# Performance work log

Hardware: AMD Instinct MI355X
Metric: run time of the kernel (lower is better)

## Reference

```python
import jax, jax.numpy as jnp
import numpy as np

B, N, D, H = 8, 8192, 512, 8  # batch, seq, hidden, heads
DH = D // H


def _rope_tables(n, d, dtype=jnp.float32):
    # standard rotate-half RoPE tables over the full hidden dim (d/2 freq pairs)
    half = d // 2
    inv_freq = 1.0 / (10000.0 ** (np.arange(0, half, dtype=np.float32) / half))
    pos = np.arange(n, dtype=np.float32)
    ang = np.einsum('n,f->nf', pos, inv_freq)          # [N, D/2]
    ang = np.concatenate([ang, ang], axis=-1)          # [N, D]
    return jnp.asarray(np.cos(ang), dtype), jnp.asarray(np.sin(ang), dtype)


def setup_inputs() -> dict:
    key = jax.random.key(0)
    k1, k2 = jax.random.split(key)
    hidden_states = jax.random.normal(k1, (B, N, D), dtype=jnp.float32)
    num_layers = 24
    std = 0.02 / np.sqrt(2.0 * num_layers * D)
    W = jax.random.normal(k2, (D, D), dtype=jnp.float32) * std
    cos, sin = _rope_tables(N, D)
    return {"hidden_states": hidden_states, "W": W, "cos": cos, "sin": sin}


def _rotate_half(x):
    x1, x2 = jnp.split(x, 2, axis=-1)
    return jnp.concatenate([-x2, x1], axis=-1)


def reference(hidden_states, W, cos, sin):
    # dropout(p=0) in eval mode -> identity
    x = hidden_states * cos + _rotate_half(hidden_states) * sin  # RoPE, [B,N,D]
    q = jnp.einsum('bnd,ed->bne', x, W)                          # F.linear(x, W)
    qh = q.reshape(B, N, H, DH)
    xh = x.reshape(B, N, H, DH)
    # linear-complexity path: (K^T V) then Q @ (.), per head
    kv = jnp.einsum('bnhd,bnhe->bhde', xh, xh)   # [B,H,DH,DH]
    out = jnp.einsum('bnhd,bhde->bnhe', qh, kv)  # [B,N,H,DH]
    return out.reshape(B, N, D)
```

## Files before the change

### kernel.cpp

```cpp
#include <hip/hip_runtime.h>
#include <hip/hip_bf16.h>
#include <stdint.h>

#define BB 8
#define NN 8192
#define DD 512
#define HH 8
#define DHD 64
#define NCH 32

typedef __attribute__((ext_vector_type(8))) short bf16x8;
typedef __attribute__((ext_vector_type(4))) float f32x4;
typedef __attribute__((ext_vector_type(4))) float f4v;

__device__ __forceinline__ unsigned short f2bf(float f) {
  union { float f; unsigned int u; } v; v.f = f;
  return (unsigned short)((v.u + 0x7FFFu + ((v.u >> 16) & 1u)) >> 16);
}

__device__ __forceinline__ void async16(const void* g, void* l) {
  __builtin_amdgcn_global_load_lds(
      (const __attribute__((address_space(1))) void*)g,
      (__attribute__((address_space(3))) void*)l, 16, 0, 0);
}

__global__ __launch_bounds__(512, 2) void ropekv_kernel(
    const float* __restrict__ h, const float* __restrict__ cs,
    const float* __restrict__ sn, unsigned short* __restrict__ x,
    float* __restrict__ kvp, int nbh) {
  __shared__ __align__(16) unsigned int xt32[2][512 * 34];
  int blk = blockIdx.x;
  int chunk = blk & 31, b = blk >> 5;
  int tid = threadIdx.x;
  int wave = tid >> 6, lane = tid & 63;
  int rpar = lane & 1;
  int g = lane >> 1;
  int cf = g * 8;
  int l15 = lane & 15, q = lane >> 4;
  int hd = wave * 64;
  size_t row0 = (size_t)b * NN + (size_t)chunk * 256;
  int n0 = chunk * 256;

  f32x4 acc[4][4];
#pragma unroll
  for (int i = 0; i < 4; ++i)
#pragma unroll
    for (int j = 0; j < 4; ++j) acc[i][j] = (f32x4){0.f, 0.f, 0.f, 0.f};

  f4v ha[2][4][2], hb[2][4][2];

  auto loadt = [&](int t) {
    int pb = t & 1;
#pragma unroll
    for (int p = 0; p < 4; ++p) {
      int r = p * 16 + wave * 2 + rpar;
      const float* hp = h + (row0 + t * 64 + r) * DD + cf;
      ha[pb][p][0] = __builtin_nontemporal_load((const f4v*)hp);
      ha[pb][p][1] = __builtin_nontemporal_load((const f4v*)(hp + 4));
      hb[pb][p][0] = __builtin_nontemporal_load((const f4v*)(hp + 256));
      hb[pb][p][1] = __builtin_nontemporal_load((const f4v*)(hp + 260));
    }
  };

  auto ropet = [&](int t) {
    int pb = t & 1;
#pragma unroll
    for (int p = 0; p < 4; ++p) {
      int r = p * 16 + wave * 2 + rpar;
      int nr = n0 + t * 64 + r;
      const float* cp = cs + (size_t)nr * DD + cf;
      const float* sp = sn + (size_t)nr * DD + cf;
      f4v c0 = *(const f4v*)cp, c1 = *(const f4v*)(cp + 4);
      f4v s0 = *(const f4v*)sp, s1 = *(const f4v*)(sp + 4);
      f4v xl0 = ha[pb][p][0] * c0 - hb[pb][p][0] * s0;
      f4v xl1 = ha[pb][p][1] * c1 - hb[pb][p][1] * s1;
      f4v xh0 = hb[pb][p][0] * c0 + ha[pb][p][0] * s0;
      f4v xh1 = hb[pb][p][1] * c1 + ha[pb][p][1] * s1;
      unsigned ml[4], mh[4];
      ml[0] = (unsigned)f2bf(xl0.x) | ((unsigned)f2bf(xl0.y) << 16);
      ml[1] = (unsigned)f2bf(xl0.z) | ((unsigned)f2bf(xl0.w) << 16);
      ml[2] = (unsigned)f2bf(xl1.x) | ((unsigned)f2bf(xl1.y) << 16);
      ml[3] = (unsigned)f2bf(xl1.z) | ((unsigned)f2bf(xl1.w) << 16);
      mh[0] = (unsigned)f2bf(xh0.x) | ((unsigned)f2bf(xh0.y) << 16);
      mh[1] = (unsigned)f2bf(xh0.z) | ((unsigned)f2bf(xh0.w) << 16);
      mh[2] = (unsigned)f2bf(xh1.x) | ((unsigned)f2bf(xh1.y) << 16);
      mh[3] = (unsigned)f2bf(xh1.z) | ((unsigned)f2bf(xh1.w) << 16);
      unsigned short* xp = x + (row0 + t * 64 + r) * DD + cf;
      uint4 st0; st0.x = ml[0]; st0.y = ml[1]; st0.z = ml[2]; st0.w = ml[3];
      uint4 st1; st1.x = mh[0]; st1.y = mh[1]; st1.z = mh[2]; st1.w = mh[3];
      *(uint4*)xp         = st0;
      *(uint4*)(xp + 256) = st1;
      unsigned pk[8];
#pragma unroll
      for (int k = 0; k < 4; ++k) {
        unsigned mine = rpar ? mh[k] : ml[k];
        unsigned send = rpar ? ml[k] : mh[k];
        unsigned recv = (unsigned)__shfl_xor((int)send, 1, 64);
        if (!rpar) {
          pk[2 * k]     = (mine & 0xffffu) | (recv << 16);
          pk[2 * k + 1] = (mine >> 16) | (recv & 0xffff0000u);
        } else {
          pk[2 * k]     = (recv & 0xffffu) | (mine << 16);
          pk[2 * k + 1] = (recv >> 16) | (mine & 0xffff0000u);
        }
      }
      int np = p * 8 + wave;
      int dbase = cf + (rpar ? 256 : 0);
      int rot = (g >> 1) & 7;
#pragma unroll
      for (int w = 0; w < 8; ++w) {
        int jj = (w + rot) & 7;
        xt32[pb][(dbase + jj) * 34 + np] = pk[jj];
      }
    }
  };

  auto mfmat = [&](int t) {
    const unsigned short* xt16 = (const unsigned short*)xt32[t & 1];
#pragma unroll
    for (int ks = 0; ks < 64; ks += 32) {
      bf16x8 af[4];
#pragma unroll
      for (int i = 0; i < 4; ++i)
        af[i] = *(const bf16x8*)&xt16[(hd + i * 16 + l15) * 68 + ks + q * 8];
#pragma unroll
      for (int i = 0; i < 4; ++i)
#pragma unroll
        for (int j = 0; j < 4; ++j)
          acc[i][j] = __builtin_amdgcn_mfma_f32_16x16x32_bf16(af[i], af[j], acc[i][j], 0, 0, 0);
    }
  };

  loadt(0);
  ropet(0);
  loadt(1);
  __syncthreads();
#pragma unroll
  for (int t = 0; t < 4; ++t) {
    if (t < 2) loadt(t + 2);
    if (t < 3) ropet(t + 1);
    mfmat(t);
    __syncthreads();
  }

  int bh = b * 8 + wave;
  float* dst = kvp + ((size_t)chunk * nbh + bh) * 4096;
#pragma unroll
  for (int i = 0; i < 4; ++i)
#pragma unroll
    for (int j = 0; j < 4; ++j)
#pragma unroll
      for (int reg = 0; reg < 4; ++reg)
        dst[(i * 16 + q * 4 + reg) * 64 + j * 16 + l15] = acc[i][j][reg];
}

__global__ __launch_bounds__(512, 2) void wkvt_kernel(
    const float* __restrict__ W, const float* __restrict__ kvp,
    unsigned short* __restrict__ wkvt, int nbh) {
  __shared__ float kvs[64 * 16];
  __shared__ __align__(16) float ws[64 * 512];
  int blk = blockIdx.x;
  int bh = blk >> 2, eq = blk & 3;
  int b = bh >> 3, hh = bh & 7;
  int tid = threadIdx.x;
  if (tid < 256) {
    int idx = tid * 4;
    int d = idx >> 4, ec = idx & 15;
    f4v s = (f4v){0.f, 0.f, 0.f, 0.f};
    for (int c = 0; c < NCH; ++c)
      s += *(const f4v*)&kvp[((size_t)c * nbh + bh) * 4096 + d * 64 + eq * 16 + ec];
    *(f4v*)&kvs[idx] = s;
  }
#pragma unroll
  for (int i = 0; i < 16; ++i) {
    int idx = i * 2048 + tid * 4;
    *(f4v*)&ws[idx] = *(const f4v*)&W[(size_t)(hh * DHD + (idx >> 9)) * DD + (idx & 511)];
  }
  __syncthreads();
  int el = tid & 15, fg = tid >> 4;
  f4v av[4];
#pragma unroll
  for (int k = 0; k < 4; ++k) av[k] = (f4v){0.f, 0.f, 0.f, 0.f};
#pragma unroll 8
  for (int d = 0; d < 64; ++d) {
    float kvv = kvs[d * 16 + el];
    const f4v* wr = (const f4v*)&ws[d * DD + fg * 16];
#pragma unroll
    for (int k = 0; k < 4; ++k) av[k] += wr[k] * kvv;
  }
  unsigned short tb[16];
#pragma unroll
  for (int k = 0; k < 4; ++k) {
    tb[k * 4 + 0] = f2bf(av[k].x); tb[k * 4 + 1] = f2bf(av[k].y);
    tb[k * 4 + 2] = f2bf(av[k].z); tb[k * 4 + 3] = f2bf(av[k].w);
  }
  size_t ob = ((size_t)b * DD + hh * DHD + eq * 16 + el) * DD + fg * 16;
  *(uint4*)&wkvt[ob]     = *(uint4*)&tb[0];
  *(uint4*)&wkvt[ob + 8] = *(uint4*)&tb[8];
}

__global__ __launch_bounds__(256, 2) void gemm_kernel(const unsigned short* __restrict__ x,
                                                      const unsigned short* __restrict__ wkvt,
                                                      float* __restrict__ out) {
  __shared__ __align__(16) unsigned short As[128 * 64];
  __shared__ __align__(16) unsigned short Bs[256 * 64];
  int mt = blockIdx.x, ct = blockIdx.y, bz = blockIdx.z;
  int tid = threadIdx.x, wave = tid >> 6, lane = tid & 63;
  int m_off = (wave & 1) * 64, c_off = (wave >> 1) * 128;
  int l15 = lane & 15, q = lane >> 4;
  int lrow = lane >> 3, lcol = (lane & 7) * 8;
  const unsigned short* Ag = x    + ((size_t)bz * NN + mt * 128) * DD;
  const unsigned short* Bg = wkvt + ((size_t)bz * DD + ct * 256) * DD;
  f32x4 acc[4][8];
#pragma unroll
  for (int i = 0; i < 4; ++i)
#pragma unroll
    for (int j = 0; j < 8; ++j) acc[i][j] = (f32x4){0.f, 0.f, 0.f, 0.f};

  for (int kk = 0; kk < 512; kk += 64) {
#pragma unroll
    for (int i = 0; i < 4; ++i)
      async16(Ag + (size_t)(wave * 32 + i * 8 + lrow) * DD + kk + lcol,
              &As[(wave * 32 + i * 8) * 64]);
#pragma unroll
    for (int i = 0; i < 8; ++i)
      async16(Bg + (size_t)(wave * 64 + i * 8 + lrow) * DD + kk + lcol,
              &Bs[(wave * 64 + i * 8) * 64]);
    __syncthreads();
#pragma unroll
    for (int ks = 0; ks < 64; ks += 32) {
      bf16x8 a[4], bb[8];
#pragma unroll
      for (int i = 0; i < 4; ++i)
        a[i] = *(const bf16x8*)&As[(m_off + i * 16 + l15) * 64 + ks + q * 8];
#pragma unroll
      for (int j = 0; j < 8; ++j)
        bb[j] = *(const bf16x8*)&Bs[(c_off + j * 16 + l15) * 64 + ks + q * 8];
#pragma unroll
      for (int i = 0; i < 4; ++i)
#pragma unroll
        for (int j = 0; j < 8; ++j)
          acc[i][j] = __builtin_amdgcn_mfma_f32_16x16x32_bf16(a[i], bb[j], acc[i][j], 0, 0, 0);
    }
    __syncthreads();
  }
  float* ob = out + ((size_t)bz * NN + mt * 128) * DD + ct * 256;
#pragma unroll
  for (int i = 0; i < 4; ++i)
#pragma unroll
    for (int j = 0; j < 8; ++j) {
      int row = m_off + i * 16 + q * 4;
      int col = c_off + j * 16 + l15;
#pragma unroll
      for (int reg = 0; reg < 4; ++reg)
        __builtin_nontemporal_store(acc[i][j][reg], &ob[(size_t)(row + reg) * DD + col]);
    }
}

extern "C" void kernel_launch(void* const* d_in, const int* in_sizes, int n_in,
                              void* d_out, int out_size, void* d_ws, size_t ws_size,
                              hipStream_t stream) {
  (void)in_sizes; (void)n_in; (void)out_size;
  const float* h  = (const float*)d_in[0];
  const float* W  = (const float*)d_in[1];
  const float* cs = (const float*)d_in[2];
  const float* sn = (const float*)d_in[3];
  float* out = (float*)d_out;

  const size_t x_full     = (size_t)BB * NN * DD * 2;
  const size_t kvp_full   = (size_t)NCH * BB * HH * DHD * DHD * 4;
  const size_t wkvt_full  = (size_t)BB * DD * DD * 2;
  const size_t x_batch    = (size_t)NN * DD * 2;
  const size_t kvp_batch  = (size_t)NCH * HH * DHD * DHD * 4;
  const size_t wkvt_batch = (size_t)DD * DD * 2;

  if (ws_size >= x_full + kvp_full + wkvt_full) {
    unsigned short* xw   = (unsigned short*)d_ws;
    float*          kvp  = (float*)((char*)d_ws + x_full);
    unsigned short* wkvt = (unsigned short*)((char*)d_ws + x_full + kvp_full);
    ropekv_kernel<<<dim3(BB * 32), dim3(512), 0, stream>>>(h, cs, sn, xw, kvp, BB * HH);
    wkvt_kernel<<<dim3(BB * HH * 4), dim3(512), 0, stream>>>(W, kvp, wkvt, BB * HH);
    gemm_kernel<<<dim3(NN / 128, DD / 256, BB), dim3(256), 0, stream>>>(xw, wkvt, out);
  } else {
    unsigned short* xw   = (unsigned short*)d_ws;
    float*          kvp  = (float*)((char*)d_ws + x_batch);
    unsigned short* wkvt = (unsigned short*)((char*)d_ws + x_batch + kvp_batch);
    for (int b = 0; b < BB; ++b) {
      ropekv_kernel<<<dim3(32), dim3(512), 0, stream>>>(
          h + (size_t)b * NN * DD, cs, sn, xw, kvp, HH);
      wkvt_kernel<<<dim3(HH * 4), dim3(512), 0, stream>>>(W, kvp, wkvt, HH);
      gemm_kernel<<<dim3(NN / 128, DD / 256, 1), dim3(256), 0, stream>>>(
          xw, wkvt, out + (size_t)b * NN * DD);
    }
  }
}
```

Before: 336.0 us.

## Split ropekv heads across two waves and shrink GEMM tile to 128x128

```diff
diff --git a/kernel.cpp b/kernel.cpp
--- a/kernel.cpp
+++ b/kernel.cpp
@@ -24,7 +24,7 @@
       (__attribute__((address_space(3))) void*)l, 16, 0, 0);
 }
 
-__global__ __launch_bounds__(512, 2) void ropekv_kernel(
+__global__ __launch_bounds__(1024, 4) void ropekv_kernel(
     const float* __restrict__ h, const float* __restrict__ cs,
     const float* __restrict__ sn, unsigned short* __restrict__ x,
     float* __restrict__ kvp, int nbh) {
@@ -37,45 +37,46 @@
   int g = lane >> 1;
   int cf = g * 8;
   int l15 = lane & 15, q = lane >> 4;
-  int hd = wave * 64;
+  int head = wave >> 1;
+  int half = wave & 1;
+  int hd = head * 64;
   size_t row0 = (size_t)b * NN + (size_t)chunk * 256;
   int n0 = chunk * 256;
 
-  f32x4 acc[4][4];
-#pragma unroll
-  for (int i = 0; i < 4; ++i)
+  f32x4 acc[2][4];
+#pragma unroll
+  for (int i = 0; i < 2; ++i)
 #pragma unroll
     for (int j = 0; j < 4; ++j) acc[i][j] = (f32x4){0.f, 0.f, 0.f, 0.f};
 
-  f4v ha[2][4][2], hb[2][4][2];
+  f4v ha[2][2], hb[2][2];
 
   auto loadt = [&](int t) {
-    int pb = t & 1;
-#pragma unroll
-    for (int p = 0; p < 4; ++p) {
-      int r = p * 16 + wave * 2 + rpar;
+#pragma unroll
+    for (int p = 0; p < 2; ++p) {
+      int r = 2 * (wave + 16 * p) + rpar;
       const float* hp = h + (row0 + t * 64 + r) * DD + cf;
-      ha[pb][p][0] = __builtin_nontemporal_load((const f4v*)hp);
-      ha[pb][p][1] = __builtin_nontemporal_load((const f4v*)(hp + 4));
-      hb[pb][p][0] = __builtin_nontemporal_load((const f4v*)(hp + 256));
-      hb[pb][p][1] = __builtin_nontemporal_load((const f4v*)(hp + 260));
+      ha[p][0] = __builtin_nontemporal_load((const f4v*)hp);
+      ha[p][1] = __builtin_nontemporal_load((const f4v*)(hp + 4));
+      hb[p][0] = __builtin_nontemporal_load((const f4v*)(hp + 256));
+      hb[p][1] = __builtin_nontemporal_load((const f4v*)(hp + 260));
     }
   };
 
   auto ropet = [&](int t) {
     int pb = t & 1;
 #pragma unroll
-    for (int p = 0; p < 4; ++p) {
-      int r = p * 16 + wave * 2 + rpar;
+    for (int p = 0; p < 2; ++p) {
+      int r = 2 * (wave + 16 * p) + rpar;
       int nr = n0 + t * 64 + r;
       const float* cp = cs + (size_t)nr * DD + cf;
       const float* sp = sn + (size_t)nr * DD + cf;
       f4v c0 = *(const f4v*)cp, c1 = *(const f4v*)(cp + 4);
       f4v s0 = *(const f4v*)sp, s1 = *(const f4v*)(sp + 4);
-      f4v xl0 = ha[pb][p][0] * c0 - hb[pb][p][0] * s0;
-      f4v xl1 = ha[pb][p][1] * c1 - hb[pb][p][1] * s1;
-      f4v xh0 = hb[pb][p][0] * c0 + ha[pb][p][0] * s0;
-      f4v xh1 = hb[pb][p][1] * c1 + ha[pb][p][1] * s1;
+      f4v xl0 = ha[p][0] * c0 - hb[p][0] * s0;
+      f4v xl1 = ha[p][1] * c1 - hb[p][1] * s1;
+      f4v xh0 = hb[p][0] * c0 + ha[p][0] * s0;
+      f4v xh1 = hb[p][1] * c1 + ha[p][1] * s1;
       unsigned ml[4], mh[4];
       ml[0] = (unsigned)f2bf(xl0.x) | ((unsigned)f2bf(xl0.y) << 16);
       ml[1] = (unsigned)f2bf(xl0.z) | ((unsigned)f2bf(xl0.w) << 16);
@@ -104,7 +105,7 @@
           pk[2 * k + 1] = (recv >> 16) | (mine & 0xffff0000u);
         }
       }
-      int np = p * 8 + wave;
+      int np = wave + 16 * p;
       int dbase = cf + (rpar ? 256 : 0);
       int rot = (g >> 1) & 7;
 #pragma unroll
@@ -119,15 +120,18 @@
     const unsigned short* xt16 = (const unsigned short*)xt32[t & 1];
 #pragma unroll
     for (int ks = 0; ks < 64; ks += 32) {
-      bf16x8 af[4];
-#pragma unroll
-      for (int i = 0; i < 4; ++i)
-        af[i] = *(const bf16x8*)&xt16[(hd + i * 16 + l15) * 68 + ks + q * 8];
-#pragma unroll
-      for (int i = 0; i < 4; ++i)
+      bf16x8 af[2], bf[4];
+#pragma unroll
+      for (int i = 0; i < 2; ++i)
+        af[i] = *(const bf16x8*)&xt16[(hd + half * 32 + i * 16 + l15) * 68 + ks + q * 8];
+#pragma unroll
+      for (int j = 0; j < 4; ++j)
+        bf[j] = *(const bf16x8*)&xt16[(hd + j * 16 + l15) * 68 + ks + q * 8];
+#pragma unroll
+      for (int i = 0; i < 2; ++i)
 #pragma unroll
         for (int j = 0; j < 4; ++j)
-          acc[i][j] = __builtin_amdgcn_mfma_f32_16x16x32_bf16(af[i], af[j], acc[i][j], 0, 0, 0);
+          acc[i][j] = __builtin_amdgcn_mfma_f32_16x16x32_bf16(af[i], bf[j], acc[i][j], 0, 0, 0);
     }
   };
 
@@ -137,21 +141,21 @@
   __syncthreads();
 #pragma unroll
   for (int t = 0; t < 4; ++t) {
+    if (t < 3) ropet(t + 1);
     if (t < 2) loadt(t + 2);
-    if (t < 3) ropet(t + 1);
     mfmat(t);
     __syncthreads();
   }
 
-  int bh = b * 8 + wave;
+  int bh = b * 8 + head;
   float* dst = kvp + ((size_t)chunk * nbh + bh) * 4096;
 #pragma unroll
-  for (int i = 0; i < 4; ++i)
+  for (int i = 0; i < 2; ++i)
 #pragma unroll
     for (int j = 0; j < 4; ++j)
 #pragma unroll
       for (int reg = 0; reg < 4; ++reg)
-        dst[(i * 16 + q * 4 + reg) * 64 + j * 16 + l15] = acc[i][j][reg];
+        dst[(half * 32 + i * 16 + q * 4 + reg) * 64 + j * 16 + l15] = acc[i][j][reg];
 }
 
 __global__ __launch_bounds__(512, 2) void wkvt_kernel(
@@ -199,23 +203,23 @@
   *(uint4*)&wkvt[ob + 8] = *(uint4*)&tb[8];
 }
 
-__global__ __launch_bounds__(256, 2) void gemm_kernel(const unsigned short* __restrict__ x,
+__global__ __launch_bounds__(256, 3) void gemm_kernel(const unsigned short* __restrict__ x,
                                                       const unsigned short* __restrict__ wkvt,
                                                       float* __restrict__ out) {
   __shared__ __align__(16) unsigned short As[128 * 64];
-  __shared__ __align__(16) unsigned short Bs[256 * 64];
+  __shared__ __align__(16) unsigned short Bs[128 * 64];
   int mt = blockIdx.x, ct = blockIdx.y, bz = blockIdx.z;
   int tid = threadIdx.x, wave = tid >> 6, lane = tid & 63;
-  int m_off = (wave & 1) * 64, c_off = (wave >> 1) * 128;
+  int wm = wave & 1, wn = wave >> 1;
   int l15 = lane & 15, q = lane >> 4;
   int lrow = lane >> 3, lcol = (lane & 7) * 8;
   const unsigned short* Ag = x    + ((size_t)bz * NN + mt * 128) * DD;
-  const unsigned short* Bg = wkvt + ((size_t)bz * DD + ct * 256) * DD;
-  f32x4 acc[4][8];
+  const unsigned short* Bg = wkvt + ((size_t)bz * DD + ct * 128) * DD;
+  f32x4 acc[4][4];
 #pragma unroll
   for (int i = 0; i < 4; ++i)
 #pragma unroll
-    for (int j = 0; j < 8; ++j) acc[i][j] = (f32x4){0.f, 0.f, 0.f, 0.f};
+    for (int j = 0; j < 4; ++j) acc[i][j] = (f32x4){0.f, 0.f, 0.f, 0.f};
 
   for (int kk = 0; kk < 512; kk += 64) {
 #pragma unroll
@@ -223,34 +227,34 @@
       async16(Ag + (size_t)(wave * 32 + i * 8 + lrow) * DD + kk + lcol,
               &As[(wave * 32 + i * 8) * 64]);
 #pragma unroll
-    for (int i = 0; i < 8; ++i)
-      async16(Bg + (size_t)(wave * 64 + i * 8 + lrow) * DD + kk + lcol,
-              &Bs[(wave * 64 + i * 8) * 64]);
+    for (int i = 0; i < 4; ++i)
+      async16(Bg + (size_t)(wave * 32 + i * 8 + lrow) * DD + kk + lcol,
+              &Bs[(wave * 32 + i * 8) * 64]);
     __syncthreads();
 #pragma unroll
     for (int ks = 0; ks < 64; ks += 32) {
-      bf16x8 a[4], bb[8];
+      bf16x8 a[4], bb[4];
 #pragma unroll
       for (int i = 0; i < 4; ++i)
-        a[i] = *(const bf16x8*)&As[(m_off + i * 16 + l15) * 64 + ks + q * 8];
-#pragma unroll
-      for (int j = 0; j < 8; ++j)
-        bb[j] = *(const bf16x8*)&Bs[(c_off + j * 16 + l15) * 64 + ks + q * 8];
+        a[i] = *(const bf16x8*)&As[(wm * 64 + i * 16 + l15) * 64 + ks + q * 8];
+#pragma unroll
+      for (int j = 0; j < 4; ++j)
+        bb[j] = *(const bf16x8*)&Bs[(wn * 64 + j * 16 + l15) * 64 + ks + q * 8];
 #pragma unroll
       for (int i = 0; i < 4; ++i)
 #pragma unroll
-        for (int j = 0; j < 8; ++j)
+        for (int j = 0; j < 4; ++j)
           acc[i][j] = __builtin_amdgcn_mfma_f32_16x16x32_bf16(a[i], bb[j], acc[i][j], 0, 0, 0);
     }
     __syncthreads();
   }
-  float* ob = out + ((size_t)bz * NN + mt * 128) * DD + ct * 256;
+  float* ob = out + ((size_t)bz * NN + mt * 128 + wm * 64) * DD + ct * 128 + wn * 64;
 #pragma unroll
   for (int i = 0; i < 4; ++i)
 #pragma unroll
-    for (int j = 0; j < 8; ++j) {
-      int row = m_off + i * 16 + q * 4;
-      int col = c_off + j * 16 + l15;
+    for (int j = 0; j < 4; ++j) {
+      int row = i * 16 + q * 4;
+      int col = j * 16 + l15;
 #pragma unroll
       for (int reg = 0; reg < 4; ++reg)
         __builtin_nontemporal_store(acc[i][j][reg], &ob[(size_t)(row + reg) * DD + col]);
@@ -278,18 +282,18 @@
     unsigned short* xw   = (unsigned short*)d_ws;
     float*          kvp  = (float*)((char*)d_ws + x_full);
     unsigned short* wkvt = (unsigned short*)((char*)d_ws + x_full + kvp_full);
-    ropekv_kernel<<<dim3(BB * 32), dim3(512), 0, stream>>>(h, cs, sn, xw, kvp, BB * HH);
+    ropekv_kernel<<<dim3(BB * 32), dim3(1024), 0, stream>>>(h, cs, sn, xw, kvp, BB * HH);
     wkvt_kernel<<<dim3(BB * HH * 4), dim3(512), 0, stream>>>(W, kvp, wkvt, BB * HH);
-    gemm_kernel<<<dim3(NN / 128, DD / 256, BB), dim3(256), 0, stream>>>(xw, wkvt, out);
+    gemm_kernel<<<dim3(NN / 128, DD / 128, BB), dim3(256), 0, stream>>>(xw, wkvt, out);
   } else {
     unsigned short* xw   = (unsigned short*)d_ws;
     float*          kvp  = (float*)((char*)d_ws + x_batch);
     unsigned short* wkvt = (unsigned short*)((char*)d_ws + x_batch + kvp_batch);
     for (int b = 0; b < BB; ++b) {
-      ropekv_kernel<<<dim3(32), dim3(512), 0, stream>>>(
+      ropekv_kernel<<<dim3(32), dim3(1024), 0, stream>>>(
           h + (size_t)b * NN * DD, cs, sn, xw, kvp, HH);
       wkvt_kernel<<<dim3(HH * 4), dim3(512), 0, stream>>>(W, kvp, wkvt, HH);
-      gemm_kernel<<<dim3(NN / 128, DD / 256, 1), dim3(256), 0, stream>>>(
+      gemm_kernel<<<dim3(NN / 128, DD / 128, 1), dim3(256), 0, stream>>>(
           xw, wkvt, out + (size_t)b * NN * DD);
     }
   }
```

Result: faster. 322.1 us (-4.2%).
